# Performance work log

Measured on AMD Instinct MI355X. Metric: run time of the kernel, lower is better.

## Reference

```python
import jax, jax.numpy as jnp
import numpy as np

LATENT = 1024
ENC = 4096
B = 8192


def setup_inputs() -> dict:
    key = jax.random.key(0)
    k1, k2, k3, k4 = jax.random.split(key, 4)
    inp = jax.random.normal(k1, (B, LATENT), dtype=jnp.float32)
    enc = jax.random.normal(k2, (B, ENC), dtype=jnp.float32)
    # nn.Linear(ENC, LATENT): weight [LATENT, ENC], bias [LATENT]
    bound = 1.0 / np.sqrt(ENC)
    W = jax.random.uniform(k3, (LATENT, ENC), minval=-bound, maxval=bound, dtype=jnp.float32)
    b = jax.random.uniform(k4, (LATENT,), minval=-bound, maxval=bound, dtype=jnp.float32)
    return {"input": inp, "encoder_output": enc, "W": W, "b": b}


def reference(input, encoder_output, W, b):
    # vector = Linear(encoder_output)  -> [B, LATENT]
    v = jnp.einsum("be,de->bd", encoder_output, W) + b
    # Fused Householder-style reflection (math identical to bmm(vv^T, x)):
    # out = x - 2 * v * (v . x) / ||v||   (original divides by norm, not norm^2)
    dot = jnp.sum(v * input, axis=1, keepdims=True)          # [B, 1]
    norm = jnp.linalg.norm(v, axis=1, keepdims=True)         # [B, 1]
    output = input - 2.0 * v * dot / norm                    # [B, LATENT]
    log_det = jnp.zeros((input.shape[0], 1), dtype=input.dtype)
    return (output, log_det)
```

## Files before the change

### kernel.cpp

```cpp
#include <hip/hip_runtime.h>
#include <hip/hip_bf16.h>
#include <stdint.h>

#define M_DIM 8192
#define N_DIM 1024
#define K_DIM 4096

typedef __bf16 bf16x8 __attribute__((ext_vector_type(8)));
typedef float f32x4 __attribute__((ext_vector_type(4)));
typedef __hip_bfloat16 bf16_t;

__device__ __forceinline__ void gload_lds16(const void* g, void* l) {
  __builtin_amdgcn_global_load_lds(
      (const __attribute__((address_space(1))) void*)g,
      (__attribute__((address_space(3))) void*)l, 16, 0, 0);
}

__global__ __launch_bounds__(256) void pack_both(const float* __restrict__ enc,
                                                 const float* __restrict__ W,
                                                 int4* __restrict__ pA,
                                                 int4* __restrict__ pB) {
  const unsigned gtid = blockIdx.x * 256 + threadIdx.x;
  const float* src;
  int4* dst;
  unsigned t;
  if (gtid < 4194304u) { src = enc; dst = pA; t = gtid; }
  else                 { src = W;   dst = pB; t = gtid - 4194304u; }
  const unsigned cp = t & 7;
  const unsigned tmp = t >> 3;
  const unsigned r = tmp & 255;
  const unsigned tmp2 = tmp >> 8;
  const unsigned kt = tmp2 & 63;
  const unsigned rt = tmp2 >> 6;
  const unsigned srow = (rt << 8) + r;
  const unsigned k0 = (kt << 6) + ((cp ^ (r & 7)) << 3);
  const float4* s = (const float4*)(src + (size_t)srow * 4096 + k0);
  float4 a = s[0], b = s[1];
  union { bf16_t h[8]; int4 v; } u;
  u.h[0] = __float2bfloat16(a.x); u.h[1] = __float2bfloat16(a.y);
  u.h[2] = __float2bfloat16(a.z); u.h[3] = __float2bfloat16(a.w);
  u.h[4] = __float2bfloat16(b.x); u.h[5] = __float2bfloat16(b.y);
  u.h[6] = __float2bfloat16(b.z); u.h[7] = __float2bfloat16(b.w);
  dst[t] = u.v;
}

__device__ __forceinline__ void stage_half(const char* g, char* smem, int ldsoff, int tid) {
  gload_lds16(g + tid * 16, smem + ldsoff + tid * 16);
  gload_lds16(g + 8192 + tid * 16, smem + ldsoff + 8192 + tid * 16);
}

__global__ __launch_bounds__(512, 2) void gemm8(
    const char* __restrict__ pA, const char* __restrict__ pB,
    float* __restrict__ V0, float* __restrict__ V1p, int NT) {
  extern __shared__ char smem[];
  const int tid = threadIdx.x;
  const int lane = tid & 63, wave = tid >> 6;
  const int wm = wave >> 2, wn = wave & 3;
  const int lrow = lane & 15, lkc = lane >> 4;

  const int cpx = (int)gridDim.x >> 3;
  const int swz = ((int)blockIdx.x & 7) * cpx + ((int)blockIdx.x >> 3);
  const int split = swz >> 7;
  const int rem = swz & 127;
  const int mt = rem >> 2, nt = rem & 3;

  const char* Abase = pA + ((size_t)mt * 64 + (size_t)split * NT) * 32768;
  const char* Bbase = pB + ((size_t)nt * 64 + (size_t)split * NT) * 32768;
  float* V = split ? V1p : V0;

  int colw[2];
  colw[0] = ((lkc) ^ (lrow & 7)) << 4;
  colw[1] = ((4 + lkc) ^ (lrow & 7)) << 4;
  int aRow[4], bRow[2];
  #pragma unroll
  for (int f = 0; f < 4; ++f) aRow[f] = (wm * 64 + f * 16 + lrow) * 128;
  #pragma unroll
  for (int f2 = 0; f2 < 2; ++f2) bRow[f2] = 32768 + (wn * 32 + f2 * 16 + lrow) * 128;

  f32x4 acc[2][4][2][2];
  #pragma unroll
  for (int a0 = 0; a0 < 2; ++a0)
    #pragma unroll
    for (int a1 = 0; a1 < 4; ++a1)
      #pragma unroll
      for (int a2 = 0; a2 < 2; ++a2)
        #pragma unroll
        for (int a3 = 0; a3 < 2; ++a3)
          acc[a0][a1][a2][a3] = (f32x4){0.f, 0.f, 0.f, 0.f};

  const int ktm = NT - 1;

  stage_half(Abase, smem, 0, tid);
  stage_half(Bbase + 16384, smem, 32768 + 16384, tid);
  stage_half(Abase + 16384, smem, 16384, tid);
  stage_half(Bbase, smem, 32768, tid);
  stage_half(Abase + 32768, smem, 65536, tid);
  stage_half(Bbase + 32768 + 16384, smem, 65536 + 32768 + 16384, tid);
  asm volatile("s_waitcnt vmcnt(4)" ::: "memory");
  __builtin_amdgcn_s_barrier();

  for (int g = 0; g < NT; ++g) {
    const int bb = g & 1, nbf = bb ^ 1;
    char* ab = smem + bb * 65536;
    const char* A1t = Abase + (size_t)((g + 1) & ktm) * 32768;
    const char* B1t = Bbase + (size_t)((g + 1) & ktm) * 32768;
    const char* A2t = Abase + (size_t)((g + 2) & ktm) * 32768;
    const char* B2t = Bbase + (size_t)((g + 2) & ktm) * 32768;

    bf16x8 a[4][2], b0[2][2], b1[2][2];

    #pragma unroll
    for (int f = 0; f < 4; ++f)
      #pragma unroll
      for (int s = 0; s < 2; ++s)
        a[f][s] = *(const bf16x8*)(ab + aRow[f] + colw[s]);
    #pragma unroll
    for (int f2 = 0; f2 < 2; ++f2)
      #pragma unroll
      for (int s = 0; s < 2; ++s)
        b0[f2][s] = *(const bf16x8*)(ab + bRow[f2] + colw[s]);
    stage_half(A1t + 16384, smem, nbf * 65536 + 16384, tid);
    __builtin_amdgcn_sched_barrier(0);
    __builtin_amdgcn_s_barrier();
    asm volatile("s_waitcnt lgkmcnt(0)" ::: "memory");
    __builtin_amdgcn_sched_barrier(0);
    __builtin_amdgcn_s_setprio(1);
    #pragma unroll
    for (int f = 0; f < 4; ++f)
      #pragma unroll
      for (int f2 = 0; f2 < 2; ++f2)
        #pragma unroll
        for (int s = 0; s < 2; ++s)
          acc[0][f][0][f2] = __builtin_amdgcn_mfma_f32_16x16x32_bf16(
              a[f][s], b0[f2][s], acc[0][f][0][f2], 0, 0, 0);
    __builtin_amdgcn_s_setprio(0);
    __builtin_amdgcn_sched_barrier(0);
    __builtin_amdgcn_s_barrier();

    #pragma unroll
    for (int f2 = 0; f2 < 2; ++f2)
      #pragma unroll
      for (int s = 0; s < 2; ++s)
        b1[f2][s] = *(const bf16x8*)(ab + bRow[f2] + 16384 + colw[s]);
    stage_half(B1t, smem, nbf * 65536 + 32768, tid);
    __builtin_amdgcn_sched_barrier(0);
    __builtin_amdgcn_s_barrier();
    asm volatile("s_waitcnt lgkmcnt(0)" ::: "memory");
    __builtin_amdgcn_sched_barrier(0);
    __builtin_amdgcn_s_setprio(1);
    #pragma unroll
    for (int f = 0; f < 4; ++f)
      #pragma unroll
      for (int f2 = 0; f2 < 2; ++f2)
        #pragma unroll
        for (int s = 0; s < 2; ++s)
          acc[0][f][1][f2] = __builtin_amdgcn_mfma_f32_16x16x32_bf16(
              a[f][s], b1[f2][s], acc[0][f][1][f2], 0, 0, 0);
    __builtin_amdgcn_s_setprio(0);
    __builtin_amdgcn_sched_barrier(0);
    __builtin_amdgcn_s_barrier();

    #pragma unroll
    for (int f = 0; f < 4; ++f)
      #pragma unroll
      for (int s = 0; s < 2; ++s)
        a[f][s] = *(const bf16x8*)(ab + aRow[f] + 16384 + colw[s]);
    stage_half(A2t, smem, bb * 65536, tid);
    __builtin_amdgcn_sched_barrier(0);
    __builtin_amdgcn_s_barrier();
    asm volatile("s_waitcnt lgkmcnt(0)" ::: "memory");
    __builtin_amdgcn_sched_barrier(0);
    __builtin_amdgcn_s_setprio(1);
    #pragma unroll
    for (int f = 0; f < 4; ++f)
      #pragma unroll
      for (int f2 = 0; f2 < 2; ++f2)
        #pragma unroll
        for (int s = 0; s < 2; ++s)
          acc[1][f][1][f2] = __builtin_amdgcn_mfma_f32_16x16x32_bf16(
              a[f][s], b1[f2][s], acc[1][f][1][f2], 0, 0, 0);
    __builtin_amdgcn_s_setprio(0);
    __builtin_amdgcn_sched_barrier(0);
    __builtin_amdgcn_s_barrier();

    stage_half(B2t + 16384, smem, bb * 65536 + 32768 + 16384, tid);
    __builtin_amdgcn_sched_barrier(0);
    __builtin_amdgcn_s_barrier();
    __builtin_amdgcn_s_setprio(1);
    #pragma unroll
    for (int f = 0; f < 4; ++f)
      #pragma unroll
      for (int f2 = 0; f2 < 2; ++f2)
        #pragma unroll
        for (int s = 0; s < 2; ++s)
          acc[1][f][0][f2] = __builtin_amdgcn_mfma_f32_16x16x32_bf16(
              a[f][s], b0[f2][s], acc[1][f][0][f2], 0, 0, 0);
    __builtin_amdgcn_s_setprio(0);
    asm volatile("s_waitcnt vmcnt(4)" ::: "memory");
    __builtin_amdgcn_sched_barrier(0);
    __builtin_amdgcn_s_barrier();
  }

  const int lq = lane >> 4;
  #pragma unroll
  for (int qm = 0; qm < 2; ++qm)
    #pragma unroll
    for (int f = 0; f < 4; ++f) {
      const int rowg = mt * 256 + qm * 128 + wm * 64 + f * 16 + lq * 4;
      #pragma unroll
      for (int reg = 0; reg < 4; ++reg) {
        float* Vr = V + (size_t)(rowg + reg) * N_DIM + nt * 256 + wn * 32 + lrow;
        #pragma unroll
        for (int qn = 0; qn < 2; ++qn)
          #pragma unroll
          for (int f2 = 0; f2 < 2; ++f2)
            Vr[qn * 128 + f2 * 16] = acc[qm][f][qn][f2][reg];
      }
    }
}

__global__ __launch_bounds__(256) void householder_ep(
    const float* __restrict__ x, const float* __restrict__ bias,
    float* __restrict__ vio, const float* __restrict__ V2,
    float* __restrict__ logdet) {
  const int row = blockIdx.x;
  const int t = threadIdx.x;
  float4* vr = (float4*)(vio + (size_t)row * N_DIM);
  const float4* xr = (const float4*)(x + (size_t)row * N_DIM);
  const float4* br = (const float4*)bias;

  float4 v = vr[t];
  if (V2) {
    float4 v2 = ((const float4*)(V2 + (size_t)row * N_DIM))[t];
    v.x += v2.x; v.y += v2.y; v.z += v2.z; v.w += v2.w;
  }
  float4 bb = br[t];
  v.x += bb.x; v.y += bb.y; v.z += bb.z; v.w += bb.w;
  float4 xx = xr[t];

  float dot = v.x * xx.x + v.y * xx.y + v.z * xx.z + v.w * xx.w;
  float nsq = v.x * v.x + v.y * v.y + v.z * v.z + v.w * v.w;

  #pragma unroll
  for (int off = 32; off > 0; off >>= 1) {
    dot += __shfl_down(dot, off);
    nsq += __shfl_down(nsq, off);
  }
  __shared__ float sd[4], sn[4];
  if ((t & 63) == 0) { sd[t >> 6] = dot; sn[t >> 6] = nsq; }
  __syncthreads();
  dot = sd[0] + sd[1] + sd[2] + sd[3];
  nsq = sn[0] + sn[1] + sn[2] + sn[3];

  const float f = 2.0f * dot / sqrtf(nsq);
  float4 o;
  o.x = xx.x - f * v.x;
  o.y = xx.y - f * v.y;
  o.z = xx.z - f * v.z;
  o.w = xx.w - f * v.w;
  vr[t] = o;
  if (t == 0) logdet[row] = 0.0f;
}

extern "C" void kernel_launch(void* const* d_in, const int* in_sizes, int n_in,
                              void* d_out, int out_size, void* d_ws, size_t ws_size,
                              hipStream_t stream) {
  const float* x   = (const float*)d_in[0];
  const float* enc = (const float*)d_in[1];
  const float* W   = (const float*)d_in[2];
  const float* b   = (const float*)d_in[3];

  float* out    = (float*)d_out;
  float* v      = out;
  float* logdet = out + (size_t)M_DIM * N_DIM;

  char*  packA = (char*)d_ws;
  char*  packB = packA + (size_t)64 * 1024 * 1024;
  float* V2    = (float*)(packB + (size_t)8 * 1024 * 1024);

  const size_t need2 = (size_t)104 * 1024 * 1024;
  const int nsplit = (ws_size >= need2) ? 2 : 1;

  pack_both<<<18432, 256, 0, stream>>>(enc, W, (int4*)packA, (int4*)packB);

  hipFuncSetAttribute((const void*)gemm8, hipFuncAttributeMaxDynamicSharedMemorySize, 131072);
  gemm8<<<dim3(128 * nsplit), 512, 131072, stream>>>(
      packA, packB, v, nsplit == 2 ? V2 : nullptr, 64 / nsplit);

  householder_ep<<<M_DIM, 256, 0, stream>>>(x, b, v, nsplit == 2 ? V2 : nullptr, logdet);
}
```

Measured before the change: 121.9 us.

## Fuse fp32-to-bf16 conversion of encoder output into GEMM A-tile loading

The encoder activations are no longer pre-packed to bf16 in a separate pass. The GEMM now loads raw fp32 rows into registers, converts them to bf16, and writes them swizzled into LDS inside the pipelined main loop. This removes a full read-and-write round trip of the 128MB A matrix and shrinks the workspace requirement. In exchange it doubles the A bytes each GEMM tile reads, adds VGPR pressure, and puts conversion ALU work and extra waitcnt hazards into the MFMA schedule.

```diff
diff --git a/kernel.cpp b/kernel.cpp
--- a/kernel.cpp
+++ b/kernel.cpp
@@ -16,16 +16,9 @@
       (__attribute__((address_space(3))) void*)l, 16, 0, 0);
 }
 
-__global__ __launch_bounds__(256) void pack_both(const float* __restrict__ enc,
-                                                 const float* __restrict__ W,
-                                                 int4* __restrict__ pA,
-                                                 int4* __restrict__ pB) {
-  const unsigned gtid = blockIdx.x * 256 + threadIdx.x;
-  const float* src;
-  int4* dst;
-  unsigned t;
-  if (gtid < 4194304u) { src = enc; dst = pA; t = gtid; }
-  else                 { src = W;   dst = pB; t = gtid - 4194304u; }
+__global__ __launch_bounds__(256) void pack_w(const float* __restrict__ W,
+                                              int4* __restrict__ pB) {
+  const unsigned t = blockIdx.x * 256 + threadIdx.x;
   const unsigned cp = t & 7;
   const unsigned tmp = t >> 3;
   const unsigned r = tmp & 255;
@@ -34,14 +27,14 @@
   const unsigned rt = tmp2 >> 6;
   const unsigned srow = (rt << 8) + r;
   const unsigned k0 = (kt << 6) + ((cp ^ (r & 7)) << 3);
-  const float4* s = (const float4*)(src + (size_t)srow * 4096 + k0);
+  const float4* s = (const float4*)(W + (size_t)srow * 4096 + k0);
   float4 a = s[0], b = s[1];
   union { bf16_t h[8]; int4 v; } u;
   u.h[0] = __float2bfloat16(a.x); u.h[1] = __float2bfloat16(a.y);
   u.h[2] = __float2bfloat16(a.z); u.h[3] = __float2bfloat16(a.w);
   u.h[4] = __float2bfloat16(b.x); u.h[5] = __float2bfloat16(b.y);
   u.h[6] = __float2bfloat16(b.z); u.h[7] = __float2bfloat16(b.w);
-  dst[t] = u.v;
+  pB[t] = u.v;
 }
 
 __device__ __forceinline__ void stage_half(const char* g, char* smem, int ldsoff, int tid) {
@@ -49,8 +42,27 @@
   gload_lds16(g + 8192 + tid * 16, smem + ldsoff + 8192 + tid * 16);
 }
 
+__device__ __forceinline__ void issue4(const float* g, float4* r) {
+  const float4* s = (const float4*)g;
+  r[0] = s[0]; r[1] = s[1]; r[2] = s[2]; r[3] = s[3];
+}
+
+__device__ __forceinline__ void cvt_write(const float4* r, char* base, int o0) {
+  union { bf16_t h[8]; int4 v; } u0, u1;
+  u0.h[0] = __float2bfloat16(r[0].x); u0.h[1] = __float2bfloat16(r[0].y);
+  u0.h[2] = __float2bfloat16(r[0].z); u0.h[3] = __float2bfloat16(r[0].w);
+  u0.h[4] = __float2bfloat16(r[1].x); u0.h[5] = __float2bfloat16(r[1].y);
+  u0.h[6] = __float2bfloat16(r[1].z); u0.h[7] = __float2bfloat16(r[1].w);
+  u1.h[0] = __float2bfloat16(r[2].x); u1.h[1] = __float2bfloat16(r[2].y);
+  u1.h[2] = __float2bfloat16(r[2].z); u1.h[3] = __float2bfloat16(r[2].w);
+  u1.h[4] = __float2bfloat16(r[3].x); u1.h[5] = __float2bfloat16(r[3].y);
+  u1.h[6] = __float2bfloat16(r[3].z); u1.h[7] = __float2bfloat16(r[3].w);
+  *(int4*)(base + o0) = u0.v;
+  *(int4*)(base + (o0 ^ 16)) = u1.v;
+}
+
 __global__ __launch_bounds__(512, 2) void gemm8(
-    const char* __restrict__ pA, const char* __restrict__ pB,
+    const float* __restrict__ Araw, const char* __restrict__ pB,
     float* __restrict__ V0, float* __restrict__ V1p, int NT) {
   extern __shared__ char smem[];
   const int tid = threadIdx.x;
@@ -64,9 +76,12 @@
   const int rem = swz & 127;
   const int mt = rem >> 2, nt = rem & 3;
 
-  const char* Abase = pA + ((size_t)mt * 64 + (size_t)split * NT) * 32768;
   const char* Bbase = pB + ((size_t)nt * 64 + (size_t)split * NT) * 32768;
   float* V = split ? V1p : V0;
+
+  const float* aG = Araw + (size_t)(mt * 256 + (tid >> 2)) * K_DIM +
+                    (size_t)split * (NT * 64) + (tid & 3) * 16;
+  const int wrO0 = (tid >> 2) * 128 + ((((tid & 3) << 1) ^ ((tid >> 2) & 7)) << 4);
 
   int colw[2];
   colw[0] = ((lkc) ^ (lrow & 7)) << 4;
@@ -89,23 +104,29 @@
           acc[a0][a1][a2][a3] = (f32x4){0.f, 0.f, 0.f, 0.f};
 
   const int ktm = NT - 1;
-
-  stage_half(Abase, smem, 0, tid);
+  float4 ga[4], gb[4];
+
+  issue4(aG, ga);
+  issue4(aG + 128 * K_DIM, gb);
+  stage_half(Bbase, smem, 32768, tid);
   stage_half(Bbase + 16384, smem, 32768 + 16384, tid);
-  stage_half(Abase + 16384, smem, 16384, tid);
-  stage_half(Bbase, smem, 32768, tid);
-  stage_half(Abase + 32768, smem, 65536, tid);
+  asm volatile("s_waitcnt vmcnt(4)" ::: "memory");
+  cvt_write(ga, smem + 0, wrO0);
+  cvt_write(gb, smem + 16384, wrO0);
+  issue4(aG + 64, ga);
+  issue4(aG + 64 + 128 * K_DIM, gb);
   stage_half(Bbase + 32768 + 16384, smem, 65536 + 32768 + 16384, tid);
-  asm volatile("s_waitcnt vmcnt(4)" ::: "memory");
+  asm volatile("s_waitcnt vmcnt(6)" ::: "memory");
+  cvt_write(ga, smem + 65536, wrO0);
+  asm volatile("s_waitcnt lgkmcnt(0)" ::: "memory");
   __builtin_amdgcn_s_barrier();
 
   for (int g = 0; g < NT; ++g) {
     const int bb = g & 1, nbf = bb ^ 1;
     char* ab = smem + bb * 65536;
-    const char* A1t = Abase + (size_t)((g + 1) & ktm) * 32768;
     const char* B1t = Bbase + (size_t)((g + 1) & ktm) * 32768;
-    const char* A2t = Abase + (size_t)((g + 2) & ktm) * 32768;
     const char* B2t = Bbase + (size_t)((g + 2) & ktm) * 32768;
+    const float* aP = aG + (size_t)((g + 2) & ktm) * 64;
 
     bf16x8 a[4][2], b0[2][2], b1[2][2];
 
@@ -119,7 +140,6 @@
       #pragma unroll
       for (int s = 0; s < 2; ++s)
         b0[f2][s] = *(const bf16x8*)(ab + bRow[f2] + colw[s]);
-    stage_half(A1t + 16384, smem, nbf * 65536 + 16384, tid);
     __builtin_amdgcn_sched_barrier(0);
     __builtin_amdgcn_s_barrier();
     asm volatile("s_waitcnt lgkmcnt(0)" ::: "memory");
@@ -134,6 +154,8 @@
           acc[0][f][0][f2] = __builtin_amdgcn_mfma_f32_16x16x32_bf16(
               a[f][s], b0[f2][s], acc[0][f][0][f2], 0, 0, 0);
     __builtin_amdgcn_s_setprio(0);
+    asm volatile("s_waitcnt vmcnt(2)" ::: "memory");
+    cvt_write(gb, smem + nbf * 65536 + 16384, wrO0);
     __builtin_amdgcn_sched_barrier(0);
     __builtin_amdgcn_s_barrier();
 
@@ -142,6 +164,7 @@
       #pragma unroll
       for (int s = 0; s < 2; ++s)
         b1[f2][s] = *(const bf16x8*)(ab + bRow[f2] + 16384 + colw[s]);
+    issue4(aP, ga);
     stage_half(B1t, smem, nbf * 65536 + 32768, tid);
     __builtin_amdgcn_sched_barrier(0);
     __builtin_amdgcn_s_barrier();
@@ -165,7 +188,6 @@
       #pragma unroll
       for (int s = 0; s < 2; ++s)
         a[f][s] = *(const bf16x8*)(ab + aRow[f] + 16384 + colw[s]);
-    stage_half(A2t, smem, bb * 65536, tid);
     __builtin_amdgcn_sched_barrier(0);
     __builtin_amdgcn_s_barrier();
     asm volatile("s_waitcnt lgkmcnt(0)" ::: "memory");
@@ -180,9 +202,12 @@
           acc[1][f][1][f2] = __builtin_amdgcn_mfma_f32_16x16x32_bf16(
               a[f][s], b1[f2][s], acc[1][f][1][f2], 0, 0, 0);
     __builtin_amdgcn_s_setprio(0);
-    __builtin_amdgcn_sched_barrier(0);
-    __builtin_amdgcn_s_barrier();
-
+    asm volatile("s_waitcnt vmcnt(2)" ::: "memory");
+    cvt_write(ga, smem + bb * 65536, wrO0);
+    __builtin_amdgcn_sched_barrier(0);
+    __builtin_amdgcn_s_barrier();
+
+    issue4(aP + 128 * K_DIM, gb);
     stage_half(B2t + 16384, smem, bb * 65536 + 32768 + 16384, tid);
     __builtin_amdgcn_sched_barrier(0);
     __builtin_amdgcn_s_barrier();
@@ -196,7 +221,7 @@
           acc[1][f][0][f2] = __builtin_amdgcn_mfma_f32_16x16x32_bf16(
               a[f][s], b0[f2][s], acc[1][f][0][f2], 0, 0, 0);
     __builtin_amdgcn_s_setprio(0);
-    asm volatile("s_waitcnt vmcnt(4)" ::: "memory");
+    asm volatile("s_waitcnt vmcnt(6)" ::: "memory");
     __builtin_amdgcn_sched_barrier(0);
     __builtin_amdgcn_s_barrier();
   }
@@ -274,18 +299,17 @@
   float* v      = out;
   float* logdet = out + (size_t)M_DIM * N_DIM;
 
-  char*  packA = (char*)d_ws;
-  char*  packB = packA + (size_t)64 * 1024 * 1024;
+  char*  packB = (char*)d_ws;
   float* V2    = (float*)(packB + (size_t)8 * 1024 * 1024);
 
-  const size_t need2 = (size_t)104 * 1024 * 1024;
+  const size_t need2 = (size_t)40 * 1024 * 1024;
   const int nsplit = (ws_size >= need2) ? 2 : 1;
 
-  pack_both<<<18432, 256, 0, stream>>>(enc, W, (int4*)packA, (int4*)packB);
+  pack_w<<<2048, 256, 0, stream>>>(W, (int4*)packB);
 
   hipFuncSetAttribute((const void*)gemm8, hipFuncAttributeMaxDynamicSharedMemorySize, 131072);
   gemm8<<<dim3(128 * nsplit), 512, 131072, stream>>>(
-      packA, packB, v, nsplit == 2 ? V2 : nullptr, 64 / nsplit);
+      enc, packB, v, nsplit == 2 ? V2 : nullptr, 64 / nsplit);
 
   householder_ep<<<M_DIM, 256, 0, stream>>>(x, b, v, nsplit == 2 ? V2 : nullptr, logdet);
 }
```

Result: faster. 113.0 us (-7.3%).

## Prefetch next-tile LDS fragments across iterations and cut barriers per k-step

Applied to the files above, without the earlier changes.

Restructures the GEMM main loop so the A-even and B0 register fragments for the next k-tile are read from LDS at the end of the current iteration. The per-phase lgkmcnt waits and extra barriers are removed, which lets LDS reads overlap with MFMA work. The global-to-LDS staging order and the vmcnt thresholds are also rearranged, so B halves are issued in pairs. In exchange it uses more registers (separate aE/aO fragment sets), and the relaxed waits raise the risk of LDS races if the counts are wrong.

```diff
diff --git a/kernel.cpp b/kernel.cpp
--- a/kernel.cpp
+++ b/kernel.cpp
@@ -90,52 +90,34 @@
 
   const int ktm = NT - 1;
 
-  stage_half(Abase, smem, 0, tid);
-  stage_half(Bbase + 16384, smem, 32768 + 16384, tid);
+  stage_half(Abase,         smem, 0, tid);
   stage_half(Abase + 16384, smem, 16384, tid);
-  stage_half(Bbase, smem, 32768, tid);
+  stage_half(Bbase,         smem, 32768, tid);
+  stage_half(Bbase + 16384, smem, 49152, tid);
   stage_half(Abase + 32768, smem, 65536, tid);
-  stage_half(Bbase + 32768 + 16384, smem, 65536 + 32768 + 16384, tid);
-  asm volatile("s_waitcnt vmcnt(4)" ::: "memory");
+  asm volatile("s_waitcnt vmcnt(2)" ::: "memory");
+  __builtin_amdgcn_sched_barrier(0);
   __builtin_amdgcn_s_barrier();
+
+  bf16x8 aE[4][2], aO[4][2], b0[2][2], b1[2][2];
+  #pragma unroll
+  for (int f = 0; f < 4; ++f)
+    #pragma unroll
+    for (int s = 0; s < 2; ++s)
+      aE[f][s] = *(const bf16x8*)(smem + aRow[f] + colw[s]);
+  #pragma unroll
+  for (int f2 = 0; f2 < 2; ++f2)
+    #pragma unroll
+    for (int s = 0; s < 2; ++s)
+      b0[f2][s] = *(const bf16x8*)(smem + bRow[f2] + colw[s]);
 
   for (int g = 0; g < NT; ++g) {
     const int bb = g & 1, nbf = bb ^ 1;
     char* ab = smem + bb * 65536;
+    char* nb = smem + nbf * 65536;
     const char* A1t = Abase + (size_t)((g + 1) & ktm) * 32768;
     const char* B1t = Bbase + (size_t)((g + 1) & ktm) * 32768;
     const char* A2t = Abase + (size_t)((g + 2) & ktm) * 32768;
-    const char* B2t = Bbase + (size_t)((g + 2) & ktm) * 32768;
-
-    bf16x8 a[4][2], b0[2][2], b1[2][2];
-
-    #pragma unroll
-    for (int f = 0; f < 4; ++f)
-      #pragma unroll
-      for (int s = 0; s < 2; ++s)
-        a[f][s] = *(const bf16x8*)(ab + aRow[f] + colw[s]);
-    #pragma unroll
-    for (int f2 = 0; f2 < 2; ++f2)
-      #pragma unroll
-      for (int s = 0; s < 2; ++s)
-        b0[f2][s] = *(const bf16x8*)(ab + bRow[f2] + colw[s]);
-    stage_half(A1t + 16384, smem, nbf * 65536 + 16384, tid);
-    __builtin_amdgcn_sched_barrier(0);
-    __builtin_amdgcn_s_barrier();
-    asm volatile("s_waitcnt lgkmcnt(0)" ::: "memory");
-    __builtin_amdgcn_sched_barrier(0);
-    __builtin_amdgcn_s_setprio(1);
-    #pragma unroll
-    for (int f = 0; f < 4; ++f)
-      #pragma unroll
-      for (int f2 = 0; f2 < 2; ++f2)
-        #pragma unroll
-        for (int s = 0; s < 2; ++s)
-          acc[0][f][0][f2] = __builtin_amdgcn_mfma_f32_16x16x32_bf16(
-              a[f][s], b0[f2][s], acc[0][f][0][f2], 0, 0, 0);
-    __builtin_amdgcn_s_setprio(0);
-    __builtin_amdgcn_sched_barrier(0);
-    __builtin_amdgcn_s_barrier();
 
     #pragma unroll
     for (int f2 = 0; f2 < 2; ++f2)
@@ -143,10 +125,25 @@
       for (int s = 0; s < 2; ++s)
         b1[f2][s] = *(const bf16x8*)(ab + bRow[f2] + 16384 + colw[s]);
     stage_half(B1t, smem, nbf * 65536 + 32768, tid);
-    __builtin_amdgcn_sched_barrier(0);
-    __builtin_amdgcn_s_barrier();
-    asm volatile("s_waitcnt lgkmcnt(0)" ::: "memory");
-    __builtin_amdgcn_sched_barrier(0);
+    stage_half(A1t + 16384, smem, nbf * 65536 + 16384, tid);
+    __builtin_amdgcn_s_setprio(1);
+    #pragma unroll
+    for (int f = 0; f < 4; ++f)
+      #pragma unroll
+      for (int f2 = 0; f2 < 2; ++f2)
+        #pragma unroll
+        for (int s = 0; s < 2; ++s)
+          acc[0][f][0][f2] = __builtin_amdgcn_mfma_f32_16x16x32_bf16(
+              aE[f][s], b0[f2][s], acc[0][f][0][f2], 0, 0, 0);
+    __builtin_amdgcn_s_setprio(0);
+    __builtin_amdgcn_sched_barrier(0);
+    __builtin_amdgcn_s_barrier();
+
+    #pragma unroll
+    for (int f = 0; f < 4; ++f)
+      #pragma unroll
+      for (int s = 0; s < 2; ++s)
+        aO[f][s] = *(const bf16x8*)(ab + aRow[f] + 16384 + colw[s]);
     __builtin_amdgcn_s_setprio(1);
     #pragma unroll
     for (int f = 0; f < 4; ++f)
@@ -155,21 +152,19 @@
         #pragma unroll
         for (int s = 0; s < 2; ++s)
           acc[0][f][1][f2] = __builtin_amdgcn_mfma_f32_16x16x32_bf16(
-              a[f][s], b1[f2][s], acc[0][f][1][f2], 0, 0, 0);
-    __builtin_amdgcn_s_setprio(0);
-    __builtin_amdgcn_sched_barrier(0);
-    __builtin_amdgcn_s_barrier();
-
-    #pragma unroll
-    for (int f = 0; f < 4; ++f)
-      #pragma unroll
-      for (int s = 0; s < 2; ++s)
-        a[f][s] = *(const bf16x8*)(ab + aRow[f] + 16384 + colw[s]);
+              aE[f][s], b1[f2][s], acc[0][f][1][f2], 0, 0, 0);
+    __builtin_amdgcn_s_setprio(0);
+    asm volatile("s_waitcnt vmcnt(2)" ::: "memory");
+    __builtin_amdgcn_sched_barrier(0);
+    __builtin_amdgcn_s_barrier();
+
+    #pragma unroll
+    for (int f = 0; f < 4; ++f)
+      #pragma unroll
+      for (int s = 0; s < 2; ++s)
+        aE[f][s] = *(const bf16x8*)(nb + aRow[f] + colw[s]);
+    stage_half(B1t + 16384, smem, nbf * 65536 + 49152, tid);
     stage_half(A2t, smem, bb * 65536, tid);
-    __builtin_amdgcn_sched_barrier(0);
-    __builtin_amdgcn_s_barrier();
-    asm volatile("s_waitcnt lgkmcnt(0)" ::: "memory");
-    __builtin_amdgcn_sched_barrier(0);
     __builtin_amdgcn_s_setprio(1);
     #pragma unroll
     for (int f = 0; f < 4; ++f)
@@ -178,14 +173,12 @@
         #pragma unroll
         for (int s = 0; s < 2; ++s)
           acc[1][f][1][f2] = __builtin_amdgcn_mfma_f32_16x16x32_bf16(
-              a[f][s], b1[f2][s], acc[1][f][1][f2], 0, 0, 0);
-    __builtin_amdgcn_s_setprio(0);
-    __builtin_amdgcn_sched_barrier(0);
-    __builtin_amdgcn_s_barrier();
-
-    stage_half(B2t + 16384, smem, bb * 65536 + 32768 + 16384, tid);
-    __builtin_amdgcn_sched_barrier(0);
-    __builtin_amdgcn_s_barrier();
+              aO[f][s], b1[f2][s], acc[1][f][1][f2], 0, 0, 0);
+    __builtin_amdgcn_s_setprio(0);
+    asm volatile("s_waitcnt vmcnt(4)" ::: "memory");
+    __builtin_amdgcn_sched_barrier(0);
+    __builtin_amdgcn_s_barrier();
+
     __builtin_amdgcn_s_setprio(1);
     #pragma unroll
     for (int f = 0; f < 4; ++f)
@@ -194,9 +187,15 @@
         #pragma unroll
         for (int s = 0; s < 2; ++s)
           acc[1][f][0][f2] = __builtin_amdgcn_mfma_f32_16x16x32_bf16(
-              a[f][s], b0[f2][s], acc[1][f][0][f2], 0, 0, 0);
-    __builtin_amdgcn_s_setprio(0);
-    asm volatile("s_waitcnt vmcnt(4)" ::: "memory");
+              aO[f][s], b0[f2][s], acc[1][f][0][f2], 0, 0, 0);
+    __builtin_amdgcn_s_setprio(0);
+    __builtin_amdgcn_sched_barrier(0);
+    #pragma unroll
+    for (int f2 = 0; f2 < 2; ++f2)
+      #pragma unroll
+      for (int s = 0; s < 2; ++s)
+        b0[f2][s] = *(const bf16x8*)(nb + bRow[f2] + colw[s]);
+    asm volatile("s_waitcnt vmcnt(2)" ::: "memory");
     __builtin_amdgcn_sched_barrier(0);
     __builtin_amdgcn_s_barrier();
   }
```

New measurement: 119.5 us. -2.0%, faster.
